# Kernel optimization log

Hardware: AMD Instinct MI355X
Metric: run time of the kernel (lower is better)

The kernel has to match this reference:

```python
import jax, jax.numpy as jnp
import numpy as np

B, S, H, NH = 4, 2048, 1024, 16
HD = H // NH

def setup_inputs() -> dict:
    key = jax.random.key(0)
    ks = jax.random.split(key, 9)
    s = 1.0 / np.sqrt(H)
    return {
        "x": jax.random.normal(ks[0], (B, S, H), dtype=jnp.float32),
        "Wq": jax.random.uniform(ks[1], (H, H), jnp.float32, -s, s),
        "bq": jax.random.uniform(ks[2], (H,), jnp.float32, -s, s),
        "Wk": jax.random.uniform(ks[3], (H, H), jnp.float32, -s, s),
        "bk": jax.random.uniform(ks[4], (H,), jnp.float32, -s, s),
        "Wv": jax.random.uniform(ks[5], (H, H), jnp.float32, -s, s),
        "bv": jax.random.uniform(ks[6], (H,), jnp.float32, -s, s),
        "Wo": jax.random.uniform(ks[7], (H, H), jnp.float32, -s, s),
        "bo": jax.random.uniform(ks[8], (H,), jnp.float32, -s, s),
    }

def reference(x, Wq, bq, Wk, bk, Wv, bv, Wo, bo):
    b, s, h = x.shape
    scale = np.sqrt(HD).astype(np.float32)
    def split_heads(t):  # [b,s,h] -> [b,nh,s,hd]
        return t.reshape(b, s, NH, HD).transpose(0, 2, 1, 3)
    Q = split_heads(x @ Wq.T + bq)
    K = split_heads(x @ Wk.T + bk)
    V = split_heads(x @ Wv.T + bv)
    scores = jnp.einsum('bnqd,bnkd->bnqk', Q, K) / scale
    weights = jax.nn.softmax(scores, axis=-1)
    attn = jnp.einsum('bnqk,bnkd->bnqd', weights, V)
    attn = attn.transpose(0, 2, 1, 3).reshape(b, s, h)
    return attn @ Wo.T + bo
```

## Files before the change

### kernel.cpp

```cpp
#include <hip/hip_runtime.h>
#include <cstdint>

#define BB 4
#define SS 2048
#define HH 1024
#define NHH 16
#define HDD 64

typedef __bf16 bf16x8 __attribute__((ext_vector_type(8)));
typedef float f32x4 __attribute__((ext_vector_type(4)));
typedef unsigned short u16x8 __attribute__((ext_vector_type(8)));

__device__ __forceinline__ unsigned short f2b(float f) {
    unsigned int u = __float_as_uint(f);
    u += 0x7fffu + ((u >> 16) & 1u);
    return (unsigned short)(u >> 16);
}

__device__ __forceinline__ void gload_lds16(const void* g, void* l) {
    __builtin_amdgcn_global_load_lds(
        (const __attribute__((address_space(1))) void*)g,
        (__attribute__((address_space(3))) void*)l, 16, 0, 0);
}

__global__ void cvt_bf16(const float* __restrict__ in,
                         unsigned short* __restrict__ out, long n) {
    long i = ((long)blockIdx.x * blockDim.x + threadIdx.x) * 4;
    long stride = (long)gridDim.x * blockDim.x * 4;
    for (; i < n; i += stride) {
        float4 v = *reinterpret_cast<const float4*>(in + i);
        ushort4 o;
        o.x = f2b(v.x); o.y = f2b(v.y); o.z = f2b(v.z); o.w = f2b(v.w);
        *reinterpret_cast<ushort4*>(out + i) = o;
    }
}

__global__ void cvt_w4(const float* __restrict__ w0, const float* __restrict__ w1,
                       const float* __restrict__ w2, const float* __restrict__ w3,
                       unsigned short* __restrict__ out) {
    const float* s = blockIdx.y == 0 ? w0 : blockIdx.y == 1 ? w1 : blockIdx.y == 2 ? w2 : w3;
    unsigned short* o = out + (size_t)blockIdx.y * ((size_t)HH * HH);
    long n = (long)HH * HH;
    long stride = (long)gridDim.x * blockDim.x * 4;
    for (long i = ((long)blockIdx.x * blockDim.x + threadIdx.x) * 4; i < n; i += stride) {
        float4 v = *reinterpret_cast<const float4*>(s + i);
        ushort4 w;
        w.x = f2b(v.x); w.y = f2b(v.y); w.z = f2b(v.z); w.w = f2b(v.w);
        *reinterpret_cast<ushort4*>(o + i) = w;
    }
}

__global__ __launch_bounds__(256) void gemm_qkv(
    const unsigned short* __restrict__ A,
    const unsigned short* __restrict__ Bqkv,
    const float* __restrict__ bq, const float* __restrict__ bk,
    const float* __restrict__ bv,
    unsigned short* __restrict__ Qo, unsigned short* __restrict__ Ko,
    unsigned short* __restrict__ Vto)
{
    __shared__ alignas(16) unsigned short Al[128][32];
    __shared__ alignas(16) unsigned short Bl[128][32];

    const int tid = threadIdx.x;
    const int lane = tid & 63;
    const int wid  = tid >> 6;
    const int wm = wid >> 1, wn = wid & 1;
    const int l15 = lane & 15, g = lane >> 4;

    const int wg = blockIdx.x;
    const int L = (wg & 7) * 192 + (wg >> 3);
    const int row0 = (L & 63) * 128;
    const int col0 = (L >> 6) * 128;
    const int nb = col0 >> 10;
    const int cbase = col0 & 1023;
    const float* bias = nb == 0 ? bq : nb == 1 ? bk : bv;
    const int K = HH;

    f32x4 acc[4][4];
#pragma unroll
    for (int i = 0; i < 4; i++)
#pragma unroll
        for (int j = 0; j < 4; j++) acc[i][j] = (f32x4)0.0f;

    const int off0 = tid * 16;
    const int r0s = off0 >> 6, cb0 = off0 & 63;
    const int off1 = off0 + 4096;
    const int r1s = off1 >> 6, cb1 = off1 & 63;

    for (int k0 = 0; k0 < K; k0 += 32) {
        const char* gA = (const char*)(A + (size_t)row0 * K + k0);
        const char* gB = (const char*)(Bqkv + (size_t)col0 * K + k0);
        char* lA = (char*)&Al[0][0] + wid * 1024;
        char* lB = (char*)&Bl[0][0] + wid * 1024;
        gload_lds16(gA + (size_t)r0s * (K * 2) + cb0, lA);
        gload_lds16(gA + (size_t)r1s * (K * 2) + cb1, lA + 4096);
        gload_lds16(gB + (size_t)r0s * (K * 2) + cb0, lB);
        gload_lds16(gB + (size_t)r1s * (K * 2) + cb1, lB + 4096);
        __syncthreads();

        bf16x8 af[4], bf[4];
#pragma unroll
        for (int i = 0; i < 4; i++)
            af[i] = *reinterpret_cast<const bf16x8*>(&Al[wm * 64 + i * 16 + l15][g * 8]);
#pragma unroll
        for (int j = 0; j < 4; j++)
            bf[j] = *reinterpret_cast<const bf16x8*>(&Bl[wn * 64 + j * 16 + l15][g * 8]);
        __builtin_amdgcn_s_setprio(1);
#pragma unroll
        for (int i = 0; i < 4; i++)
#pragma unroll
            for (int j = 0; j < 4; j++)
                acc[i][j] = __builtin_amdgcn_mfma_f32_16x16x32_bf16(af[i], bf[j], acc[i][j], 0, 0, 0);
        __builtin_amdgcn_s_setprio(0);
        __syncthreads();
    }

#pragma unroll
    for (int i = 0; i < 4; i++) {
#pragma unroll
        for (int j = 0; j < 4; j++) {
#pragma unroll
            for (int r = 0; r < 4; r++) {
                int row = row0 + wm * 64 + i * 16 + g * 4 + r;
                int col = cbase + wn * 64 + j * 16 + l15;
                float v = acc[i][j][r] + bias[col];
                if (nb == 0) {
                    Qo[(size_t)row * HH + col] = f2b(v);
                } else if (nb == 1) {
                    Ko[(size_t)row * HH + col] = f2b(v);
                } else {
                    int b = row >> 11;
                    int s = row & (SS - 1);
                    int s6 = s & 63;
                    int sp6 = (s6 & 0x23) | ((s6 & 0x0C) << 1) | ((s6 & 0x10) >> 2);
                    int head = col >> 6;
                    int d = col & (HDD - 1);
                    size_t idx = (((size_t)b * NHH + head) * HDD + d) * SS + (s & ~63) + sp6;
                    Vto[idx] = f2b(v);
                }
            }
        }
    }
}

__global__ __launch_bounds__(256) void gemm_out(
    const unsigned short* __restrict__ A,
    const unsigned short* __restrict__ Bm,
    const float* __restrict__ bias,
    float* __restrict__ Cout,
    int M, int N, int K)
{
    __shared__ alignas(16) unsigned short Al[128][32];
    __shared__ alignas(16) unsigned short Bl[128][32];

    const int tid = threadIdx.x;
    const int lane = tid & 63;
    const int wid  = tid >> 6;
    const int wm = wid >> 1, wn = wid & 1;
    const int l15 = lane & 15, g = lane >> 4;

    const int wg = blockIdx.x;
    const int L = (wg & 7) * 64 + (wg >> 3);
    const int row0 = (L & 63) * 128;
    const int col0 = (L >> 6) * 128;

    f32x4 acc[4][4];
#pragma unroll
    for (int i = 0; i < 4; i++)
#pragma unroll
        for (int j = 0; j < 4; j++) acc[i][j] = (f32x4)0.0f;

    const int off0 = tid * 16;
    const int r0s = off0 >> 6, cb0 = off0 & 63;
    const int off1 = off0 + 4096;
    const int r1s = off1 >> 6, cb1 = off1 & 63;

    for (int k0 = 0; k0 < K; k0 += 32) {
        const char* gA = (const char*)(A + (size_t)row0 * K + k0);
        const char* gB = (const char*)(Bm + (size_t)col0 * K + k0);
        char* lA = (char*)&Al[0][0] + wid * 1024;
        char* lB = (char*)&Bl[0][0] + wid * 1024;
        gload_lds16(gA + (size_t)r0s * (K * 2) + cb0, lA);
        gload_lds16(gA + (size_t)r1s * (K * 2) + cb1, lA + 4096);
        gload_lds16(gB + (size_t)r0s * (K * 2) + cb0, lB);
        gload_lds16(gB + (size_t)r1s * (K * 2) + cb1, lB + 4096);
        __syncthreads();

        bf16x8 af[4], bf[4];
#pragma unroll
        for (int i = 0; i < 4; i++)
            af[i] = *reinterpret_cast<const bf16x8*>(&Al[wm * 64 + i * 16 + l15][g * 8]);
#pragma unroll
        for (int j = 0; j < 4; j++)
            bf[j] = *reinterpret_cast<const bf16x8*>(&Bl[wn * 64 + j * 16 + l15][g * 8]);
        __builtin_amdgcn_s_setprio(1);
#pragma unroll
        for (int i = 0; i < 4; i++)
#pragma unroll
            for (int j = 0; j < 4; j++)
                acc[i][j] = __builtin_amdgcn_mfma_f32_16x16x32_bf16(af[i], bf[j], acc[i][j], 0, 0, 0);
        __builtin_amdgcn_s_setprio(0);
        __syncthreads();
    }

#pragma unroll
    for (int i = 0; i < 4; i++) {
#pragma unroll
        for (int j = 0; j < 4; j++) {
#pragma unroll
            for (int r = 0; r < 4; r++) {
                int row = row0 + wm * 64 + i * 16 + g * 4 + r;
                int col = col0 + wn * 64 + j * 16 + l15;
                Cout[(size_t)row * N + col] = acc[i][j][r] + bias[col];
            }
        }
    }
}

__global__ __launch_bounds__(256, 4) void attn_kernel(
    const unsigned short* __restrict__ Q,
    const unsigned short* __restrict__ K,
    const unsigned short* __restrict__ Vt,
    unsigned short* __restrict__ Oa)
{
    __shared__ alignas(16) unsigned short Kf[2][8][64][8];
    __shared__ alignas(16) unsigned short Vf[2][8][64][8];

    const int tid = threadIdx.x;
    const int lane = tid & 63;
    const int wid  = tid >> 6;
    const int l15 = lane & 15, g = lane >> 4;

    const int wg = blockIdx.x;
    const int L = (wg & 7) * 128 + (wg >> 3);
    const int qt = L & 15;
    const int bh = L >> 4;
    const int b  = bh >> 4;
    const int h  = bh & 15;
    const int q0 = qt * 128;
    const int qA = q0 + wid * 32;

    const float qs = 0.125f * 1.44269504088896f;
    const unsigned short* qpA = Q + (size_t)(b * SS + qA + l15) * HH + h * HDD + g * 8;
    const unsigned short* qpB = qpA + (size_t)16 * HH;
    u16x8 ra0 = *reinterpret_cast<const u16x8*>(qpA);
    u16x8 ra1 = *reinterpret_cast<const u16x8*>(qpA + 32);
    u16x8 rb0 = *reinterpret_cast<const u16x8*>(qpB);
    u16x8 rb1 = *reinterpret_cast<const u16x8*>(qpB + 32);
#pragma unroll
    for (int j = 0; j < 8; j++) {
        ra0[j] = f2b(__uint_as_float((unsigned)ra0[j] << 16) * qs);
        ra1[j] = f2b(__uint_as_float((unsigned)ra1[j] << 16) * qs);
        rb0[j] = f2b(__uint_as_float((unsigned)rb0[j] << 16) * qs);
        rb1[j] = f2b(__uint_as_float((unsigned)rb1[j] << 16) * qs);
    }
    const bf16x8 qa0 = __builtin_bit_cast(bf16x8, ra0);
    const bf16x8 qa1 = __builtin_bit_cast(bf16x8, ra1);
    const bf16x8 qb0 = __builtin_bit_cast(bf16x8, rb0);
    const bf16x8 qb1 = __builtin_bit_cast(bf16x8, rb1);

    u16x8 ou;
#pragma unroll
    for (int j = 0; j < 8; j++) ou[j] = 0x3F80;
    const bf16x8 ones8 = __builtin_bit_cast(bf16x8, ou);
    const f32x4 zero4 = (f32x4)0.0f;

    f32x4 acc_a[4], acc_b[4];
#pragma unroll
    for (int dn = 0; dn < 4; dn++) { acc_a[dn] = zero4; acc_b[dn] = zero4; }
    float m_a = -INFINITY, m_b = -INFINITY, l_a = 0.f, l_b = 0.f;

    const int srow = tid >> 2;
    const int d0a  = (tid & 3) * 2;
    const int sfrag = ((srow >> 4) << 1) + (d0a >> 2);
    const int sslot = (srow & 15) | ((d0a & 3) << 4);

    const unsigned short* gK = K  + (size_t)(b * SS + srow) * HH + h * HDD + d0a * 8;
    const unsigned short* gV = Vt + (((size_t)b * NHH + h) * HDD + srow) * SS + d0a * 8;

    int4 kr0, kr1, vr0, vr1;

    auto stage_write = [&](int buf) {
        unsigned short* pk = &Kf[buf][sfrag][0][0] + sslot * 8;
        unsigned short* pv = &Vf[buf][sfrag][0][0] + sslot * 8;
        *reinterpret_cast<int4*>(pk)       = kr0;
        *reinterpret_cast<int4*>(pk + 128) = kr1;
        *reinterpret_cast<int4*>(pv)       = vr0;
        *reinterpret_cast<int4*>(pv + 128) = vr1;
    };

    kr0 = *reinterpret_cast<const int4*>(gK);
    kr1 = *reinterpret_cast<const int4*>(gK + 8);
    vr0 = *reinterpret_cast<const int4*>(gV);
    vr1 = *reinterpret_cast<const int4*>(gV + 8);
    stage_write(0);
    gK += (size_t)64 * HH;
    gV += 64;
    __syncthreads();

    const int NT = SS / 64;
    int cur = 0;

    for (int kt = 0; kt < NT; kt++) {
        if (kt + 1 < NT) {
            kr0 = *reinterpret_cast<const int4*>(gK);
            kr1 = *reinterpret_cast<const int4*>(gK + 8);
            vr0 = *reinterpret_cast<const int4*>(gV);
            vr1 = *reinterpret_cast<const int4*>(gV + 8);
            gK += (size_t)64 * HH;
            gV += 64;
        }

        f32x4 sa[4], sb[4];
        __builtin_amdgcn_s_setprio(1);
#pragma unroll
        for (int n = 0; n < 4; n++) {
            bf16x8 kf0 = *reinterpret_cast<const bf16x8*>(&Kf[cur][n * 2 + 0][lane][0]);
            bf16x8 kf1 = *reinterpret_cast<const bf16x8*>(&Kf[cur][n * 2 + 1][lane][0]);
            sa[n] = __builtin_amdgcn_mfma_f32_16x16x32_bf16(kf0, qa0, zero4, 0, 0, 0);
            sa[n] = __builtin_amdgcn_mfma_f32_16x16x32_bf16(kf1, qa1, sa[n], 0, 0, 0);
            sb[n] = __builtin_amdgcn_mfma_f32_16x16x32_bf16(kf0, qb0, zero4, 0, 0, 0);
            sb[n] = __builtin_amdgcn_mfma_f32_16x16x32_bf16(kf1, qb1, sb[n], 0, 0, 0);
        }
        __builtin_amdgcn_s_setprio(0);

        bf16x8 pa0, pa1, pb0, pb1;
        {
            float u0 = fmaxf(fmaxf(sa[0][0], sa[0][1]), fmaxf(sa[0][2], sa[0][3]));
            float u1 = fmaxf(fmaxf(sa[1][0], sa[1][1]), fmaxf(sa[1][2], sa[1][3]));
            float u2 = fmaxf(fmaxf(sa[2][0], sa[2][1]), fmaxf(sa[2][2], sa[2][3]));
            float u3 = fmaxf(fmaxf(sa[3][0], sa[3][1]), fmaxf(sa[3][2], sa[3][3]));
            float mt = fmaxf(fmaxf(u0, u1), fmaxf(u2, u3));
            mt = fmaxf(mt, __shfl_xor(mt, 16));
            mt = fmaxf(mt, __shfl_xor(mt, 32));
            if (!__all(mt - m_a <= 8.0f)) {
                float mnew = fmaxf(m_a, mt);
                float scl = __builtin_amdgcn_exp2f(m_a - mnew);
                m_a = mnew; l_a *= scl;
#pragma unroll
                for (int dn = 0; dn < 4; dn++)
#pragma unroll
                    for (int r = 0; r < 4; r++) acc_a[dn][r] *= scl;
            }
            float p[4][4];
#pragma unroll
            for (int n = 0; n < 4; n++)
#pragma unroll
                for (int r = 0; r < 4; r++) p[n][r] = __builtin_amdgcn_exp2f(sa[n][r] - m_a);
#pragma unroll
            for (int j = 0; j < 8; j++) {
                pa0[j] = (__bf16)p[j >> 2][j & 3];
                pa1[j] = (__bf16)p[2 + (j >> 2)][j & 3];
            }
        }
        {
            float u0 = fmaxf(fmaxf(sb[0][0], sb[0][1]), fmaxf(sb[0][2], sb[0][3]));
            float u1 = fmaxf(fmaxf(sb[1][0], sb[1][1]), fmaxf(sb[1][2], sb[1][3]));
            float u2 = fmaxf(fmaxf(sb[2][0], sb[2][1]), fmaxf(sb[2][2], sb[2][3]));
            float u3 = fmaxf(fmaxf(sb[3][0], sb[3][1]), fmaxf(sb[3][2], sb[3][3]));
            float mt = fmaxf(fmaxf(u0, u1), fmaxf(u2, u3));
            mt = fmaxf(mt, __shfl_xor(mt, 16));
            mt = fmaxf(mt, __shfl_xor(mt, 32));
            if (!__all(mt - m_b <= 8.0f)) {
                float mnew = fmaxf(m_b, mt);
                float scl = __builtin_amdgcn_exp2f(m_b - mnew);
                m_b = mnew; l_b *= scl;
#pragma unroll
                for (int dn = 0; dn < 4; dn++)
#pragma unroll
                    for (int r = 0; r < 4; r++) acc_b[dn][r] *= scl;
            }
            float p[4][4];
#pragma unroll
            for (int n = 0; n < 4; n++)
#pragma unroll
                for (int r = 0; r < 4; r++) p[n][r] = __builtin_amdgcn_exp2f(sb[n][r] - m_b);
#pragma unroll
            for (int j = 0; j < 8; j++) {
                pb0[j] = (__bf16)p[j >> 2][j & 3];
                pb1[j] = (__bf16)p[2 + (j >> 2)][j & 3];
            }
        }

        f32x4 la = zero4, lb = zero4;
        __builtin_amdgcn_s_setprio(1);
#pragma unroll
        for (int ks = 0; ks < 2; ks++) {
            bf16x8 pA = ks ? pa1 : pa0;
            bf16x8 pB = ks ? pb1 : pb0;
#pragma unroll
            for (int dn = 0; dn < 4; dn++) {
                bf16x8 vf = *reinterpret_cast<const bf16x8*>(&Vf[cur][dn * 2 + ks][lane][0]);
                acc_a[dn] = __builtin_amdgcn_mfma_f32_16x16x32_bf16(vf, pA, acc_a[dn], 0, 0, 0);
                acc_b[dn] = __builtin_amdgcn_mfma_f32_16x16x32_bf16(vf, pB, acc_b[dn], 0, 0, 0);
            }
        }
        la = __builtin_amdgcn_mfma_f32_16x16x32_bf16(ones8, pa0, la, 0, 0, 0);
        la = __builtin_amdgcn_mfma_f32_16x16x32_bf16(ones8, pa1, la, 0, 0, 0);
        lb = __builtin_amdgcn_mfma_f32_16x16x32_bf16(ones8, pb0, lb, 0, 0, 0);
        lb = __builtin_amdgcn_mfma_f32_16x16x32_bf16(ones8, pb1, lb, 0, 0, 0);
        __builtin_amdgcn_s_setprio(0);
        l_a += la[0];
        l_b += lb[0];

        if (kt + 1 < NT) stage_write(cur ^ 1);
        __syncthreads();
        cur ^= 1;
    }

    float inv_a = 1.0f / l_a;
    float inv_b = 1.0f / l_b;
    unsigned short* oA = Oa + (size_t)(b * SS + qA + l15) * HH + h * HDD;
    unsigned short* oB = oA + (size_t)16 * HH;
#pragma unroll
    for (int dn = 0; dn < 4; dn++) {
        ushort4 wa, wb;
        wa.x = f2b(acc_a[dn][0] * inv_a); wa.y = f2b(acc_a[dn][1] * inv_a);
        wa.z = f2b(acc_a[dn][2] * inv_a); wa.w = f2b(acc_a[dn][3] * inv_a);
        wb.x = f2b(acc_b[dn][0] * inv_b); wb.y = f2b(acc_b[dn][1] * inv_b);
        wb.z = f2b(acc_b[dn][2] * inv_b); wb.w = f2b(acc_b[dn][3] * inv_b);
        *reinterpret_cast<ushort4*>(oA + dn * 16 + g * 4) = wa;
        *reinterpret_cast<ushort4*>(oB + dn * 16 + g * 4) = wb;
    }
}

extern "C" void kernel_launch(void* const* d_in, const int* in_sizes, int n_in,
                              void* d_out, int out_size, void* d_ws, size_t ws_size,
                              hipStream_t stream) {
    const float* x  = (const float*)d_in[0];
    const float* Wq = (const float*)d_in[1];
    const float* bq = (const float*)d_in[2];
    const float* Wk = (const float*)d_in[3];
    const float* bk = (const float*)d_in[4];
    const float* Wv = (const float*)d_in[5];
    const float* bv = (const float*)d_in[6];
    const float* Wo = (const float*)d_in[7];
    const float* bo = (const float*)d_in[8];
    float* out = (float*)d_out;

    const int M = BB * SS;
    const long nx = (long)M * HH;

    unsigned char* ws = (unsigned char*)d_ws;
    unsigned short* xb  = (unsigned short*)(ws);
    unsigned short* Wqb = (unsigned short*)(ws + 16777216);
    unsigned short* Wob = (unsigned short*)(ws + 16777216 + 3 * 2097152);
    unsigned short* Qb  = (unsigned short*)(ws + 16777216 + 4 * 2097152);
    unsigned short* Kb  = (unsigned short*)(ws + 2 * 16777216 + 4 * 2097152);
    unsigned short* Vtb = (unsigned short*)(ws + 3 * 16777216 + 4 * 2097152);
    unsigned short* Ab  = (unsigned short*)(ws + 4 * 16777216 + 4 * 2097152);

    cvt_bf16<<<4096, 256, 0, stream>>>(x, xb, nx);
    cvt_w4<<<dim3(256, 4), 256, 0, stream>>>(Wq, Wk, Wv, Wo, Wqb);

    gemm_qkv<<<1536, 256, 0, stream>>>(xb, Wqb, bq, bk, bv, Qb, Kb, Vtb);

    attn_kernel<<<1024, 256, 0, stream>>>(Qb, Kb, Vtb, Ab);

    gemm_out<<<512, 256, 0, stream>>>(Ab, Wob, bo, out, M, HH, HH);
}
```

Baseline: 241.3 us.

## Double-buffer LDS tiles in projection GEMMs and remap block tile order

Both the QKV and output-projection GEMMs now keep two LDS buffers and issue the next k-tile's global-to-LDS loads before computing on the current tile, so memory latency can overlap MFMA work. Only one barrier per iteration remains. The block-to-tile mapping is also changed to group tiles per XCD-like partition, aiming for better L2 reuse. The setprio hints are removed. The cost is twice the LDS per block, which may reduce occupancy.

```diff
diff --git a/kernel.cpp b/kernel.cpp
--- a/kernel.cpp
+++ b/kernel.cpp
@@ -58,8 +58,8 @@
     unsigned short* __restrict__ Qo, unsigned short* __restrict__ Ko,
     unsigned short* __restrict__ Vto)
 {
-    __shared__ alignas(16) unsigned short Al[128][32];
-    __shared__ alignas(16) unsigned short Bl[128][32];
+    __shared__ alignas(16) unsigned short Al[2][128][32];
+    __shared__ alignas(16) unsigned short Bl[2][128][32];
 
     const int tid = threadIdx.x;
     const int lane = tid & 63;
@@ -68,9 +68,10 @@
     const int l15 = lane & 15, g = lane >> 4;
 
     const int wg = blockIdx.x;
-    const int L = (wg & 7) * 192 + (wg >> 3);
-    const int row0 = (L & 63) * 128;
-    const int col0 = (L >> 6) * 128;
+    const int x = wg & 7;
+    const int local = wg >> 3;
+    const int row0 = ((x & 3) * 16 + local / 12) * 128;
+    const int col0 = ((x >> 2) * 12 + local % 12) * 128;
     const int nb = col0 >> 10;
     const int cbase = col0 & 1023;
     const float* bias = nb == 0 ? bq : nb == 1 ? bk : bv;
@@ -83,36 +84,45 @@
         for (int j = 0; j < 4; j++) acc[i][j] = (f32x4)0.0f;
 
     const int off0 = tid * 16;
-    const int r0s = off0 >> 6, cb0 = off0 & 63;
+    const int aoff0 = (off0 >> 6) * (K * 2) + (off0 & 63);
     const int off1 = off0 + 4096;
-    const int r1s = off1 >> 6, cb1 = off1 & 63;
-
-    for (int k0 = 0; k0 < K; k0 += 32) {
-        const char* gA = (const char*)(A + (size_t)row0 * K + k0);
-        const char* gB = (const char*)(Bqkv + (size_t)col0 * K + k0);
-        char* lA = (char*)&Al[0][0] + wid * 1024;
-        char* lB = (char*)&Bl[0][0] + wid * 1024;
-        gload_lds16(gA + (size_t)r0s * (K * 2) + cb0, lA);
-        gload_lds16(gA + (size_t)r1s * (K * 2) + cb1, lA + 4096);
-        gload_lds16(gB + (size_t)r0s * (K * 2) + cb0, lB);
-        gload_lds16(gB + (size_t)r1s * (K * 2) + cb1, lB + 4096);
-        __syncthreads();
+    const int aoff1 = (off1 >> 6) * (K * 2) + (off1 & 63);
+
+    const char* gAb = (const char*)(A + (size_t)row0 * K);
+    const char* gBb = (const char*)(Bqkv + (size_t)col0 * K);
+
+    auto STAGE = [&](int buf, int k0) {
+        const char* a = gAb + k0 * 64;
+        const char* bsrc = gBb + k0 * 64;
+        char* lA = (char*)&Al[buf][0][0] + wid * 1024;
+        char* lB = (char*)&Bl[buf][0][0] + wid * 1024;
+        gload_lds16(a + aoff0, lA);
+        gload_lds16(a + aoff1, lA + 4096);
+        gload_lds16(bsrc + aoff0, lB);
+        gload_lds16(bsrc + aoff1, lB + 4096);
+    };
+
+    STAGE(0, 0);
+    __syncthreads();
+    int cur = 0;
+
+    for (int k = 0; k < 32; k++) {
+        if (k + 1 < 32) STAGE(cur ^ 1, k + 1);
 
         bf16x8 af[4], bf[4];
 #pragma unroll
         for (int i = 0; i < 4; i++)
-            af[i] = *reinterpret_cast<const bf16x8*>(&Al[wm * 64 + i * 16 + l15][g * 8]);
+            af[i] = *reinterpret_cast<const bf16x8*>(&Al[cur][wm * 64 + i * 16 + l15][g * 8]);
 #pragma unroll
         for (int j = 0; j < 4; j++)
-            bf[j] = *reinterpret_cast<const bf16x8*>(&Bl[wn * 64 + j * 16 + l15][g * 8]);
-        __builtin_amdgcn_s_setprio(1);
+            bf[j] = *reinterpret_cast<const bf16x8*>(&Bl[cur][wn * 64 + j * 16 + l15][g * 8]);
 #pragma unroll
         for (int i = 0; i < 4; i++)
 #pragma unroll
             for (int j = 0; j < 4; j++)
                 acc[i][j] = __builtin_amdgcn_mfma_f32_16x16x32_bf16(af[i], bf[j], acc[i][j], 0, 0, 0);
-        __builtin_amdgcn_s_setprio(0);
         __syncthreads();
+        cur ^= 1;
     }
 
 #pragma unroll
@@ -150,8 +160,8 @@
     float* __restrict__ Cout,
     int M, int N, int K)
 {
-    __shared__ alignas(16) unsigned short Al[128][32];
-    __shared__ alignas(16) unsigned short Bl[128][32];
+    __shared__ alignas(16) unsigned short Al[2][128][32];
+    __shared__ alignas(16) unsigned short Bl[2][128][32];
 
     const int tid = threadIdx.x;
     const int lane = tid & 63;
@@ -160,9 +170,10 @@
     const int l15 = lane & 15, g = lane >> 4;
 
     const int wg = blockIdx.x;
-    const int L = (wg & 7) * 64 + (wg >> 3);
-    const int row0 = (L & 63) * 128;
-    const int col0 = (L >> 6) * 128;
+    const int x = wg & 7;
+    const int local = wg >> 3;
+    const int row0 = (x * 8 + local / 8) * 128;
+    const int col0 = (local % 8) * 128;
 
     f32x4 acc[4][4];
 #pragma unroll
@@ -171,36 +182,45 @@
         for (int j = 0; j < 4; j++) acc[i][j] = (f32x4)0.0f;
 
     const int off0 = tid * 16;
-    const int r0s = off0 >> 6, cb0 = off0 & 63;
+    const int aoff0 = (off0 >> 6) * (K * 2) + (off0 & 63);
     const int off1 = off0 + 4096;
-    const int r1s = off1 >> 6, cb1 = off1 & 63;
-
-    for (int k0 = 0; k0 < K; k0 += 32) {
-        const char* gA = (const char*)(A + (size_t)row0 * K + k0);
-        const char* gB = (const char*)(Bm + (size_t)col0 * K + k0);
-        char* lA = (char*)&Al[0][0] + wid * 1024;
-        char* lB = (char*)&Bl[0][0] + wid * 1024;
-        gload_lds16(gA + (size_t)r0s * (K * 2) + cb0, lA);
-        gload_lds16(gA + (size_t)r1s * (K * 2) + cb1, lA + 4096);
-        gload_lds16(gB + (size_t)r0s * (K * 2) + cb0, lB);
-        gload_lds16(gB + (size_t)r1s * (K * 2) + cb1, lB + 4096);
-        __syncthreads();
+    const int aoff1 = (off1 >> 6) * (K * 2) + (off1 & 63);
+
+    const char* gAb = (const char*)(A + (size_t)row0 * K);
+    const char* gBb = (const char*)(Bm + (size_t)col0 * K);
+
+    auto STAGE = [&](int buf, int k0) {
+        const char* a = gAb + k0 * 64;
+        const char* bsrc = gBb + k0 * 64;
+        char* lA = (char*)&Al[buf][0][0] + wid * 1024;
+        char* lB = (char*)&Bl[buf][0][0] + wid * 1024;
+        gload_lds16(a + aoff0, lA);
+        gload_lds16(a + aoff1, lA + 4096);
+        gload_lds16(bsrc + aoff0, lB);
+        gload_lds16(bsrc + aoff1, lB + 4096);
+    };
+
+    STAGE(0, 0);
+    __syncthreads();
+    int cur = 0;
+
+    for (int k = 0; k < 32; k++) {
+        if (k + 1 < 32) STAGE(cur ^ 1, k + 1);
 
         bf16x8 af[4], bf[4];
 #pragma unroll
         for (int i = 0; i < 4; i++)
-            af[i] = *reinterpret_cast<const bf16x8*>(&Al[wm * 64 + i * 16 + l15][g * 8]);
+            af[i] = *reinterpret_cast<const bf16x8*>(&Al[cur][wm * 64 + i * 16 + l15][g * 8]);
 #pragma unroll
         for (int j = 0; j < 4; j++)
-            bf[j] = *reinterpret_cast<const bf16x8*>(&Bl[wn * 64 + j * 16 + l15][g * 8]);
-        __builtin_amdgcn_s_setprio(1);
+            bf[j] = *reinterpret_cast<const bf16x8*>(&Bl[cur][wn * 64 + j * 16 + l15][g * 8]);
 #pragma unroll
         for (int i = 0; i < 4; i++)
 #pragma unroll
             for (int j = 0; j < 4; j++)
                 acc[i][j] = __builtin_amdgcn_mfma_f32_16x16x32_bf16(af[i], bf[j], acc[i][j], 0, 0, 0);
-        __builtin_amdgcn_s_setprio(0);
         __syncthreads();
+        cur ^= 1;
     }
 
 #pragma unroll
```

Measured after the change: 234.0 us. 3.0% less time.
